# Performance work log

Hardware: AMD Instinct MI355X
Metric: run time of the kernel (lower is better)

The kernel has to match this reference:

```python
import jax, jax.numpy as jnp
import numpy as np

K = 20
EPS_BN = 1e-5

def knn_idx(x, k):
    # x: [B,N,C] -> k nearest neighbor indices [B,N,k] (self included, as in DGCNN)
    sq = jnp.sum(x * x, axis=-1)                       # [B,N]
    inner = jnp.einsum('bnc,bmc->bnm', x, x)           # [B,N,N]
    neg_dist = 2.0 * inner - sq[:, :, None] - sq[:, None, :]
    _, idx = jax.lax.top_k(neg_dist, k)
    return jax.lax.stop_gradient(idx)

def edge_feat(x, idx):
    # x: [B,N,C], idx: [B,N,k] -> [B,N,k,2C] = cat([x_j - x_i, x_i])
    nbr = jax.vmap(lambda xb, ib: xb[ib])(x, idx)      # [B,N,k,C]
    ctr = jnp.broadcast_to(x[:, :, None, :], nbr.shape)
    return jnp.concatenate([nbr - ctr, ctr], axis=-1)

def edge_conv(x, W, g, b, k):
    e = edge_feat(x, knn_idx(x, k))                    # dynamic kNN graph per layer
    h = jnp.einsum('bnkc,cd->bnkd', e, W)              # 1x1 conv2d
    h = h * (g / jnp.sqrt(1.0 + EPS_BN)) + b           # BN eval (mean=0, var=1)
    return jnp.max(jax.nn.leaky_relu(h, 0.2), axis=2)  # max over neighbors -> [B,N,d]

def layer_norm(x, g, b):
    m = jnp.mean(x, axis=-1, keepdims=True)
    v = jnp.var(x, axis=-1, keepdims=True)
    return (x - m) * jax.lax.rsqrt(v + 1e-5) * g + b

def setup_inputs():
    key = jax.random.key(0)
    B, N = 2, 4096
    ks = jax.random.split(key, 16)
    w = lambda i, shape: jax.random.normal(ks[i], shape, jnp.float32) * 0.05
    ones = lambda d: jnp.ones((d,), jnp.float32)
    zeros = lambda d: jnp.zeros((d,), jnp.float32)
    return dict(
        xyz=jax.random.normal(ks[0], (N, 3), jnp.float32),
        scale=jax.random.normal(ks[1], (N, 3), jnp.float32),
        rot=jax.random.normal(ks[2], (N, 4), jnp.float32),
        opacity=jax.random.normal(ks[3], (N, 1), jnp.float32),
        color=jax.random.normal(ks[4], (N, 3), jnp.float32),
        pose=jax.random.normal(ks[5], (B, 75), jnp.float32),
        lbs_weights=jax.random.normal(ks[6], (N, 24), jnp.float32),
        Wc1=w(7, (226, 64)), g1=ones(64), b1=zeros(64),
        Wc2=w(8, (128, 64)), g2=ones(64), b2=zeros(64),
        Wc3=w(9, (128, 128)), g3=ones(128), b3=zeros(128),
        Wc4=w(10, (256, 256)), g4=ones(256), b4=zeros(256),
        Wc5=w(11, (512, 128)), g5=ones(128), b5=zeros(128),
        Wo1=w(12, (128, 128)), bo1=zeros(128), lg1=ones(128), lb1=zeros(128),
        Wo2=w(13, (128, 128)), bo2=zeros(128), lg2=ones(128), lb2=zeros(128),
        Wo3=w(14, (128, 38)), bo3=zeros(38),
    )

def reference(xyz, scale, rot, opacity, color, pose, lbs_weights,
              Wc1, g1, b1, Wc2, g2, b2, Wc3, g3, b3, Wc4, g4, b4, Wc5, g5, b5,
              Wo1, bo1, lg1, lb1, Wo2, bo2, lg2, lb2, Wo3, bo3):
    B, N = pose.shape[0], xyz.shape[0]
    gfeat = jnp.concatenate([xyz, scale, rot, opacity, color], axis=-1)   # [N,14]
    feats = jnp.concatenate([
        jnp.broadcast_to(gfeat[None], (B, N, gfeat.shape[-1])),
        jnp.broadcast_to(lbs_weights[None], (B, N, lbs_weights.shape[-1])),
        jnp.broadcast_to(pose[:, None, :], (B, N, pose.shape[-1])),
    ], axis=-1)                                                            # [B,N,113]
    # DGCNN graph encoder (dynamic kNN EdgeConv stack)
    x1 = edge_conv(feats, Wc1, g1, b1, K)   # [B,N,64]
    x2 = edge_conv(x1, Wc2, g2, b2, K)      # [B,N,64]
    x3 = edge_conv(x2, Wc3, g3, b3, K)      # [B,N,128]
    x4 = edge_conv(x3, Wc4, g4, b4, K)      # [B,N,256]
    cat = jnp.concatenate([x1, x2, x3, x4], axis=-1)                      # [B,N,512]
    gf = jax.nn.leaky_relu(
        jnp.einsum('bnc,cd->bnd', cat, Wc5) * (g5 / jnp.sqrt(1.0 + EPS_BN)) + b5, 0.2)
    # offset predictor MLP
    h = jax.nn.leaky_relu(layer_norm(gf @ Wo1 + bo1, lg1, lb1), 0.2)
    h = jax.nn.leaky_relu(layer_norm(h @ Wo2 + bo2, lg2, lb2), 0.2)
    off = h @ Wo3 + bo3                                                   # [B,N,38]
    # residual add of gaussian offsets (first 14 dims), lbs offsets raw (last 24)
    out = jnp.concatenate([gfeat[None] + off[..., :14], off[..., 14:]], axis=-1)
    return out                                                            # [B,N,38]
```

## Files before the change

kernel.cpp:

```cpp
#include <hip/hip_runtime.h>
#include <math.h>

#define KNN 20
#define BN_INV 0.9999950000374997f

__device__ __forceinline__ unsigned f2o(float f){
    unsigned u = __float_as_uint(f);
    return (u >> 31) ? ~u : (u | 0x80000000u);
}
__device__ __forceinline__ float o2f(unsigned u){
    return __uint_as_float((u >> 31) ? (u & 0x7fffffffu) : ~u);
}
__device__ __forceinline__ float leaky(float v){ return v > 0.f ? v : 0.2f * v; }

__global__ __launch_bounds__(128) void build_feats_kernel(
    const float* __restrict__ xyz, const float* __restrict__ scale,
    const float* __restrict__ rot, const float* __restrict__ opac,
    const float* __restrict__ color, const float* __restrict__ pose,
    const float* __restrict__ lbs, float* __restrict__ feats,
    float* __restrict__ sqout, int N)
{
    __shared__ float sred[2];
    int row = blockIdx.x;
    int b = row / N, n = row % N;
    int c = threadIdx.x;
    float v = 0.f;
    if      (c <   3) v = xyz  [n*3 + c];
    else if (c <   6) v = scale[n*3 + c-3];
    else if (c <  10) v = rot  [n*4 + c-6];
    else if (c <  11) v = opac [n];
    else if (c <  14) v = color[n*3 + c-11];
    else if (c <  38) v = lbs  [n*24 + c-14];
    else if (c < 113) v = pose [b*75 + c-38];
    if (c < 116) feats[(long)row*116 + c] = v;
    float ss = v * v;
    #pragma unroll
    for (int off = 32; off; off >>= 1) ss += __shfl_xor(ss, off);
    if ((c & 63) == 0) sred[c >> 6] = ss;
    __syncthreads();
    if (c == 0) sqout[row] = sred[0] + sred[1];
}


template<int C>
__global__ __launch_bounds__(256) void dist_gemm_kernel(
    const float* __restrict__ x, int N, int CP, float* __restrict__ G)
{
    __shared__ __align__(16) float xi[128][68];
    __shared__ __align__(16) float xj[128][68];
    const int b  = blockIdx.z;
    const int bi = blockIdx.x * 128;
    const int bj = blockIdx.y * 128;
    const int t  = threadIdx.x;
    const int tx = t & 15, ty = t >> 4;
    const int CP4 = CP / 4;
    const long base = (long)b * N;
    const float4* xp = (const float4*)x;

    float acc[8][8] = {};

    for (int c0 = 0; c0 < C; c0 += 64){
        const int KCc = (C - c0 < 64) ? (C - c0) : 64;
        const int KC4 = KCc >> 2;
        __syncthreads();
        for (int f = t; f < 128 * KC4; f += 256){
            int r = f / KC4, c4 = f - r * KC4;
            float4 a = xp[(base + bi + r) * CP4 + (c0 >> 2) + c4];
            float4 bv = xp[(base + bj + r) * CP4 + (c0 >> 2) + c4];
            *(float4*)&xi[r][c4 * 4] = a;
            *(float4*)&xj[r][c4 * 4] = bv;
        }
        __syncthreads();
        for (int c = 0; c < KCc; c += 4){
            float4 A[8], Bv[8];
            #pragma unroll
            for (int ii = 0; ii < 8; ++ii) A[ii]  = *(const float4*)&xi[ty + 16*ii][c];
            #pragma unroll
            for (int jj = 0; jj < 8; ++jj) Bv[jj] = *(const float4*)&xj[tx + 16*jj][c];
            #pragma unroll
            for (int ii = 0; ii < 8; ++ii)
                #pragma unroll
                for (int jj = 0; jj < 8; ++jj){
                    acc[ii][jj] = fmaf(A[ii].x, Bv[jj].x, acc[ii][jj]);
                    acc[ii][jj] = fmaf(A[ii].y, Bv[jj].y, acc[ii][jj]);
                    acc[ii][jj] = fmaf(A[ii].z, Bv[jj].z, acc[ii][jj]);
                    acc[ii][jj] = fmaf(A[ii].w, Bv[jj].w, acc[ii][jj]);
                }
        }
    }

    #pragma unroll
    for (int ii = 0; ii < 8; ++ii){
        long rbase = (base + bi + ty + 16*ii) * N + bj;
        #pragma unroll
        for (int jj = 0; jj < 8; ++jj)
            G[rbase + tx + 16*jj] = acc[ii][jj];
    }
}

#define TCAP 256
__global__ __launch_bounds__(256) void topk_kernel(
    const float* __restrict__ G, const float* __restrict__ sq,
    int N, int* __restrict__ idx_out)
{
    __shared__ unsigned smax[256];
    __shared__ unsigned cand_u[TCAP];
    __shared__ int      cand_j[TCAP];
    __shared__ unsigned cand_cnt;
    __shared__ unsigned sTu;

    const int row = blockIdx.x;
    const int b   = row >> 12;
    const int t   = threadIdx.x;
    const float4* g4  = (const float4*)(G  + (long)row * 4096);
    const float4* sq4 = (const float4*)(sq + (long)b   * 4096);

    unsigned u[16];
    #pragma unroll
    for (int qq = 0; qq < 4; ++qq){
        int v4 = t + 256 * qq;
        float4 gg = g4[v4];
        float4 ss = sq4[v4];
        u[4*qq+0] = f2o(fmaf(2.f, gg.x, -ss.x));
        u[4*qq+1] = f2o(fmaf(2.f, gg.y, -ss.y));
        u[4*qq+2] = f2o(fmaf(2.f, gg.z, -ss.z));
        u[4*qq+3] = f2o(fmaf(2.f, gg.w, -ss.w));
    }

    unsigned mu = u[0];
    #pragma unroll
    for (int q = 1; q < 16; ++q) mu = u[q] > mu ? u[q] : mu;
    smax[t] = mu;
    if (t == 0) cand_cnt = 0;
    __syncthreads();

    int rank = 0;
    for (int k = 0; k < 256; ++k){
        unsigned ou = smax[k];
        rank += (ou > mu) || (ou == mu && k < t);
    }
    if (rank == KNN - 1) sTu = mu;
    __syncthreads();
    const unsigned Tu = sTu;

    #pragma unroll
    for (int qq = 0; qq < 4; ++qq)
        #pragma unroll
        for (int m = 0; m < 4; ++m){
            int q = 4*qq + m;
            if (u[q] >= Tu){
                unsigned p = atomicAdd(&cand_cnt, 1u);
                if (p < TCAP){ cand_u[p] = u[q]; cand_j[p] = 4*(t + 256*qq) + m; }
            }
        }
    __syncthreads();
    const int cc = (int)cand_cnt;

    if (cc <= TCAP){
        if (t < cc){
            unsigned cu = cand_u[t]; int cj = cand_j[t];
            int r = 0;
            for (int k = 0; k < cc; ++k){
                unsigned ou = cand_u[k];
                r += (ou > cu) || (ou == cu && cand_j[k] < cj);
            }
            if (r < KNN) idx_out[(long)row * KNN + r] = cj;
        }
    } else {
        __shared__ unsigned rv[4]; __shared__ int ri[4]; __shared__ int gj_;
        unsigned lv = 0u; int lj = 0x7fffffff;
        #pragma unroll
        for (int q = 0; q < 16; ++q)
            if (u[q] > lv){ lv = u[q]; lj = 4*(t + 256*(q>>2)) + (q&3); }
        for (int it = 0; it < KNN; ++it){
            unsigned bv = lv; int bj = lj;
            #pragma unroll
            for (int off = 32; off; off >>= 1){
                unsigned ov = __shfl_xor(bv, off);
                int      oj = __shfl_xor(bj, off);
                if (ov > bv || (ov == bv && oj < bj)){ bv = ov; bj = oj; }
            }
            if ((t & 63) == 0){ rv[t >> 6] = bv; ri[t >> 6] = bj; }
            __syncthreads();
            if (t == 0){
                unsigned fv = rv[0]; int fj = ri[0];
                #pragma unroll
                for (int w = 1; w < 4; ++w)
                    if (rv[w] > fv || (rv[w] == fv && ri[w] < fj)){ fv = rv[w]; fj = ri[w]; }
                gj_ = fj;
                idx_out[(long)row * KNN + it] = fj;
            }
            __syncthreads();
            int fj = gj_;
            if (fj >= 0 && ((fj >> 2) & 255) == t){
                u[((fj >> 10) << 2) | (fj & 3)] = 0u;
                lv = 0u; lj = 0x7fffffff;
                #pragma unroll
                for (int q = 0; q < 16; ++q)
                    if (u[q] > lv){ lv = u[q]; lj = 4*(t + 256*(q>>2)) + (q&3); }
            }
            __syncthreads();
        }
    }
}


__global__ void prep_wcat_kernel(const float* __restrict__ W, int C, int CP, int D,
                                 float* __restrict__ Wcat)
{
    int i = blockIdx.x * 256 + threadIdx.x;
    int TWOD = 2 * D;
    if (i >= CP * TWOD) return;
    int c = i / TWOD, n = i - c * TWOD;
    float v = 0.f;
    if (c < C) v = (n < D) ? W[c*D + n] : (W[(C + c)*D + (n - D)] - W[c*D + (n - D)]);
    Wcat[i] = v;
}

__global__ __launch_bounds__(256) void gemm_pq_kernel(
    const float* __restrict__ X, int CP, const float* __restrict__ Wcat,
    const float* __restrict__ g, const float* __restrict__ bias,
    int D, int TWOD, float* __restrict__ PQ)
{
    __shared__ __align__(16) float As[128][68];
    __shared__ __align__(16) float Bs[64][132];
    const int bi = blockIdx.x * 128;
    const int bn = blockIdx.y * 128;
    const int t  = threadIdx.x;
    const int tx = t & 15, ty = t >> 4;
    const int CP4 = CP / 4;
    const float4* xp = (const float4*)X;

    float acc[8][8] = {};

    for (int c0 = 0; c0 < CP; c0 += 64){
        const int KC = (CP - c0 < 64) ? (CP - c0) : 64;
        const int KC4 = KC >> 2;
        __syncthreads();
        for (int f = t; f < 128 * KC4; f += 256){
            int r = f / KC4, c4 = f - r * KC4;
            *(float4*)&As[r][c4 * 4] = xp[(long)(bi + r) * CP4 + (c0 >> 2) + c4];
        }
        for (int f = t; f < KC * 32; f += 256){
            int r = f >> 5, c4 = f & 31;
            *(float4*)&Bs[r][c4 * 4] = *(const float4*)&Wcat[(long)(c0 + r) * TWOD + bn + c4 * 4];
        }
        __syncthreads();
        for (int c = 0; c < KC; c += 4){
            float4 A[8];
            #pragma unroll
            for (int ii = 0; ii < 8; ++ii) A[ii] = *(const float4*)&As[ty + 16*ii][c];
            float Bv0[8], Bv1[8], Bv2[8], Bv3[8];
            #pragma unroll
            for (int jj = 0; jj < 8; ++jj){
                Bv0[jj] = Bs[c+0][tx + 16*jj];
                Bv1[jj] = Bs[c+1][tx + 16*jj];
                Bv2[jj] = Bs[c+2][tx + 16*jj];
                Bv3[jj] = Bs[c+3][tx + 16*jj];
            }
            #pragma unroll
            for (int ii = 0; ii < 8; ++ii)
                #pragma unroll
                for (int jj = 0; jj < 8; ++jj){
                    acc[ii][jj] = fmaf(A[ii].x, Bv0[jj], acc[ii][jj]);
                    acc[ii][jj] = fmaf(A[ii].y, Bv1[jj], acc[ii][jj]);
                    acc[ii][jj] = fmaf(A[ii].z, Bv2[jj], acc[ii][jj]);
                    acc[ii][jj] = fmaf(A[ii].w, Bv3[jj], acc[ii][jj]);
                }
        }
    }

    #pragma unroll
    for (int jj = 0; jj < 8; ++jj){
        int n = bn + tx + 16*jj;
        int d = (n < D) ? n : n - D;
        float gg = g[d] * BN_INV;
        float bb = (n < D) ? 0.f : bias[d];
        #pragma unroll
        for (int ii = 0; ii < 8; ++ii)
            PQ[(long)(bi + ty + 16*ii) * TWOD + n] = fmaf(acc[ii][jj], gg, bb);
    }
}

template<int D, int RPB>
__global__ __launch_bounds__(256) void gather_max_kernel(
    const float* __restrict__ PQ, const int* __restrict__ idx, int N,
    float* __restrict__ y, float* __restrict__ sqout)
{
    __shared__ int   lidx[RPB][KNN];
    __shared__ float sred[4];
    const int rb = blockIdx.x * RPB;
    const int t  = threadIdx.x;
    if (t < RPB * KNN) lidx[t / KNN][t % KNN] = idx[(long)rb * KNN + t];
    __syncthreads();

    const int r = t / D, d = t - r * D;
    const int row = rb + r;
    const long base = (long)(row / N) * N;
    const int TWOD = 2 * D;

    float q = PQ[(long)row * TWOD + D + d];
    float m = -INFINITY;
    #pragma unroll
    for (int k = 0; k < KNN; ++k){
        int j = lidx[r][k];
        m = fmaxf(m, PQ[(base + j) * TWOD + d]);
    }
    float val = leaky(m + q);
    y[(long)row * D + d] = val;

    float ss = val * val;
    #pragma unroll
    for (int off = 32; off; off >>= 1) ss += __shfl_xor(ss, off);
    if ((t & 63) == 0) sred[t >> 6] = ss;
    __syncthreads();
    if (d == 0){
        constexpr int WPR = D / 64;
        float s = 0.f;
        int w0 = (r * D) >> 6;
        #pragma unroll
        for (int w = 0; w < WPR; ++w) s += sred[w0 + w];
        sqout[row] = s;
    }
}

__global__ __launch_bounds__(256) void knn_kernel(
    const float* __restrict__ x, int N, int CP4, int* __restrict__ idx_out)
{
    __shared__ float4 xi4[32];
    __shared__ float drow[4096];
    __shared__ float rv[4];
    __shared__ int   ri[4];

    int row = blockIdx.x;
    int b = row / N;
    int t = threadIdx.x;
    const float4* xp = (const float4*)x;

    if (t < CP4) xi4[t] = xp[(long)row * CP4 + t];
    __syncthreads();

    long bb = (long)b * N * CP4;
    for (int j = t; j < N; j += 256){
        const float4* p = xp + bb + (long)j * CP4;
        float acc = 0.f;
        #pragma unroll 4
        for (int c = 0; c < CP4; ++c){
            float4 xv = p[c], yv = xi4[c];
            float dx = xv.x - yv.x, dy = xv.y - yv.y;
            float dz = xv.z - yv.z, dw = xv.w - yv.w;
            acc += dx*dx + dy*dy + dz*dz + dw*dw;
        }
        drow[j] = -acc;
    }
    __syncthreads();

    for (int it = 0; it < KNN; ++it){
        float bv = -INFINITY; int bi = N;
        for (int j = t; j < N; j += 256){
            float v = drow[j];
            if (v > bv){ bv = v; bi = j; }
        }
        #pragma unroll
        for (int off = 32; off > 0; off >>= 1){
            float ov = __shfl_xor(bv, off);
            int   oi = __shfl_xor(bi, off);
            if (ov > bv || (ov == bv && oi < bi)){ bv = ov; bi = oi; }
        }
        if ((t & 63) == 0){ rv[t >> 6] = bv; ri[t >> 6] = bi; }
        __syncthreads();
        if (t == 0){
            float fv = rv[0]; int fi = ri[0];
            #pragma unroll
            for (int w = 1; w < 4; ++w){
                if (rv[w] > fv || (rv[w] == fv && ri[w] < fi)){ fv = rv[w]; fi = ri[w]; }
            }
            idx_out[(long)row * KNN + it] = fi;
            drow[fi] = -INFINITY;
        }
        __syncthreads();
    }
}

template<int D, int KPT>
__global__ __launch_bounds__(256) void edge_conv_kernel(
    const float* __restrict__ x, int N, int C, int CP,
    const float* __restrict__ W, const float* __restrict__ g,
    const float* __restrict__ bias, const int* __restrict__ idx,
    float* __restrict__ y, float* __restrict__ sqout)
{
    __shared__ float xi[128];
    __shared__ float nbr[KNN * 128];
    __shared__ float t2[D];
    __shared__ unsigned um[D];
    __shared__ float sred[4];

    int row = blockIdx.x;
    int b = row / N;
    int t = threadIdx.x;

    for (int c = t; c < C; c += 256) xi[c] = x[(long)row * CP + c];
    for (int kk = 0; kk < KNN; ++kk){
        int j = idx[(long)row * KNN + kk];
        long nb = ((long)b * N + j) * CP;
        for (int c = t; c < C; c += 256) nbr[kk * C + c] = x[nb + c];
    }
    __syncthreads();

    for (int d = t; d < D; d += 256){
        float s = 0.f;
        for (int c = 0; c < C; ++c) s += xi[c] * W[(C + c) * D + d];
        t2[d] = s; um[d] = 0u;
    }
    __syncthreads();

    const int d  = t % D;
    const int kg = t / D;
    float s[KPT];
    #pragma unroll
    for (int q = 0; q < KPT; ++q) s[q] = t2[d];

    const float* nb0 = &nbr[(kg * KPT) * C];
    for (int c = 0; c < C; ++c){
        float w   = W[c * D + d];
        float xic = xi[c];
        #pragma unroll
        for (int q = 0; q < KPT; ++q)
            s[q] += (nb0[q * C + c] - xic) * w;
    }
    float g_ = g[d] * BN_INV, b_ = bias[d];
    float m = -INFINITY;
    #pragma unroll
    for (int q = 0; q < KPT; ++q)
        m = fmaxf(m, leaky(s[q] * g_ + b_));
    atomicMax(&um[d], f2o(m));
    __syncthreads();

    float ss = 0.f;
    for (int dd = t; dd < D; dd += 256){
        float val = o2f(um[dd]);
        y[(long)row * D + dd] = val;
        ss += val * val;
    }
    #pragma unroll
    for (int off = 32; off; off >>= 1) ss += __shfl_xor(ss, off);
    if ((t & 63) == 0) sred[t >> 6] = ss;
    __syncthreads();
    if (t == 0) sqout[row] = sred[0] + sred[1] + sred[2] + sred[3];
}

__global__ __launch_bounds__(128) void head_kernel(
    const float* __restrict__ x1, const float* __restrict__ x2,
    const float* __restrict__ x3, const float* __restrict__ x4,
    const float* __restrict__ feats,
    const float* __restrict__ Wc5, const float* __restrict__ g5, const float* __restrict__ b5,
    const float* __restrict__ Wo1, const float* __restrict__ bo1,
    const float* __restrict__ lg1, const float* __restrict__ lb1,
    const float* __restrict__ Wo2, const float* __restrict__ bo2,
    const float* __restrict__ lg2, const float* __restrict__ lb2,
    const float* __restrict__ Wo3, const float* __restrict__ bo3,
    float* __restrict__ out, int N)
{
    __shared__ float cat[512];
    __shared__ float a[128];
    __shared__ float red[128];
    __shared__ float stats[2];

    int row = blockIdx.x;
    int t = threadIdx.x;

    cat[t]       = (t < 64) ? x1[(long)row*64 + t] : x2[(long)row*64 + (t-64)];
    cat[128 + t] = x3[(long)row*128 + t];
    cat[256 + t] = x4[(long)row*256 + t];
    cat[384 + t] = x4[(long)row*256 + 128 + t];
    __syncthreads();

    float s = 0.f;
    for (int c = 0; c < 512; ++c) s += cat[c] * Wc5[c*128 + t];
    a[t] = leaky(s * g5[t] * BN_INV + b5[t]);
    __syncthreads();

    for (int layer = 0; layer < 2; ++layer){
        const float* W  = layer ? Wo2 : Wo1;
        const float* bo = layer ? bo2 : bo1;
        const float* lg = layer ? lg2 : lg1;
        const float* lb = layer ? lb2 : lb1;
        s = bo[t];
        for (int c = 0; c < 128; ++c) s += a[c] * W[c*128 + t];
        red[t] = s; __syncthreads();
        for (int st = 64; st > 0; st >>= 1){
            if (t < st) red[t] += red[t + st];
            __syncthreads();
        }
        if (t == 0) stats[0] = red[0] * (1.f/128.f);
        __syncthreads();
        float m = stats[0];
        float dm = s - m;
        red[t] = dm * dm; __syncthreads();
        for (int st = 64; st > 0; st >>= 1){
            if (t < st) red[t] += red[t + st];
            __syncthreads();
        }
        if (t == 0) stats[1] = red[0] * (1.f/128.f);
        __syncthreads();
        float var = stats[1];
        float hn = leaky(dm * rsqrtf(var + 1e-5f) * lg[t] + lb[t]);
        __syncthreads();
        a[t] = hn;
        __syncthreads();
    }

    if (t < 38){
        float o = bo3[t];
        for (int c = 0; c < 128; ++c) o += a[c] * Wo3[c*38 + t];
        if (t < 14) o += feats[(long)row*116 + t];
        out[(long)row*38 + t] = o;
    }
}

extern "C" void kernel_launch(void* const* d_in, const int* in_sizes, int n_in,
                              void* d_out, int out_size, void* d_ws, size_t ws_size,
                              hipStream_t stream)
{
    const float* xyz  = (const float*)d_in[0];
    const float* scal = (const float*)d_in[1];
    const float* rot  = (const float*)d_in[2];
    const float* opac = (const float*)d_in[3];
    const float* colr = (const float*)d_in[4];
    const float* pose = (const float*)d_in[5];
    const float* lbs  = (const float*)d_in[6];
    const float* Wc1 = (const float*)d_in[7];  const float* g1 = (const float*)d_in[8];  const float* b1 = (const float*)d_in[9];
    const float* Wc2 = (const float*)d_in[10]; const float* g2 = (const float*)d_in[11]; const float* b2 = (const float*)d_in[12];
    const float* Wc3 = (const float*)d_in[13]; const float* g3 = (const float*)d_in[14]; const float* b3 = (const float*)d_in[15];
    const float* Wc4 = (const float*)d_in[16]; const float* g4 = (const float*)d_in[17]; const float* b4 = (const float*)d_in[18];
    const float* Wc5 = (const float*)d_in[19]; const float* g5 = (const float*)d_in[20]; const float* b5 = (const float*)d_in[21];
    const float* Wo1 = (const float*)d_in[22]; const float* bo1 = (const float*)d_in[23];
    const float* lg1 = (const float*)d_in[24]; const float* lb1 = (const float*)d_in[25];
    const float* Wo2 = (const float*)d_in[26]; const float* bo2 = (const float*)d_in[27];
    const float* lg2 = (const float*)d_in[28]; const float* lb2 = (const float*)d_in[29];
    const float* Wo3 = (const float*)d_in[30]; const float* bo3 = (const float*)d_in[31];

    const int N = in_sizes[0] / 3;
    const int B = in_sizes[5] / 75;
    const int R = B * N;

    char* ws = (char*)d_ws;
    size_t o = 0;
    float* feats = (float*)(ws + o); o += (size_t)R * 116 * 4;
    float* x1    = (float*)(ws + o); o += (size_t)R * 64  * 4;
    float* x2    = (float*)(ws + o); o += (size_t)R * 64  * 4;
    float* x3    = (float*)(ws + o); o += (size_t)R * 128 * 4;
    float* x4    = (float*)(ws + o); o += (size_t)R * 256 * 4;
    int*   idx   = (int*)  (ws + o); o += (size_t)R * KNN * 4;
    float* sq    = (float*)(ws + o); o += (size_t)R * 4;
    float* Wcat  = (float*)(ws + o); o += (size_t)128 * 512 * 4;
    float* G     = (float*)(ws + o);
    float* PQ    = G;
    size_t need  = o + (size_t)B * N * N * 4;

    const bool fast = (N == 4096) && (ws_size >= need);

    build_feats_kernel<<<R, 128, 0, stream>>>(xyz, scal, rot, opac, colr, pose, lbs, feats, sq, N);

    if (fast){
        dim3 gg(N/128, N/128, B);

        dist_gemm_kernel<116><<<gg, 256, 0, stream>>>(feats, N, 116, G);
        topk_kernel<<<R, 256, 0, stream>>>(G, sq, N, idx);
        prep_wcat_kernel<<<(116*128 + 255)/256, 256, 0, stream>>>(Wc1, 113, 116, 64, Wcat);
        gemm_pq_kernel<<<dim3(R/128, 1), 256, 0, stream>>>(feats, 116, Wcat, g1, b1, 64, 128, PQ);
        gather_max_kernel<64, 4><<<R/4, 256, 0, stream>>>(PQ, idx, N, x1, sq);

        dist_gemm_kernel<64><<<gg, 256, 0, stream>>>(x1, N, 64, G);
        topk_kernel<<<R, 256, 0, stream>>>(G, sq, N, idx);
        prep_wcat_kernel<<<(64*128 + 255)/256, 256, 0, stream>>>(Wc2, 64, 64, 64, Wcat);
        gemm_pq_kernel<<<dim3(R/128, 1), 256, 0, stream>>>(x1, 64, Wcat, g2, b2, 64, 128, PQ);
        gather_max_kernel<64, 4><<<R/4, 256, 0, stream>>>(PQ, idx, N, x2, sq);

        dist_gemm_kernel<64><<<gg, 256, 0, stream>>>(x2, N, 64, G);
        topk_kernel<<<R, 256, 0, stream>>>(G, sq, N, idx);
        prep_wcat_kernel<<<(64*256 + 255)/256, 256, 0, stream>>>(Wc3, 64, 64, 128, Wcat);
        gemm_pq_kernel<<<dim3(R/128, 2), 256, 0, stream>>>(x2, 64, Wcat, g3, b3, 128, 256, PQ);
        gather_max_kernel<128, 2><<<R/2, 256, 0, stream>>>(PQ, idx, N, x3, sq);

        dist_gemm_kernel<128><<<gg, 256, 0, stream>>>(x3, N, 128, G);
        topk_kernel<<<R, 256, 0, stream>>>(G, sq, N, idx);
        prep_wcat_kernel<<<(128*512 + 255)/256, 256, 0, stream>>>(Wc4, 128, 128, 256, Wcat);
        gemm_pq_kernel<<<dim3(R/128, 4), 256, 0, stream>>>(x3, 128, Wcat, g4, b4, 256, 512, PQ);
        gather_max_kernel<256, 1><<<R, 256, 0, stream>>>(PQ, idx, N, x4, sq);
    } else {
        knn_kernel<<<R, 256, 0, stream>>>(feats, N, 116/4, idx);
        edge_conv_kernel<64, 5><<<R, 256, 0, stream>>>(feats, N, 113, 116, Wc1, g1, b1, idx, x1, sq);
        knn_kernel<<<R, 256, 0, stream>>>(x1, N, 64/4, idx);
        edge_conv_kernel<64, 5><<<R, 256, 0, stream>>>(x1, N, 64, 64, Wc2, g2, b2, idx, x2, sq);
        knn_kernel<<<R, 256, 0, stream>>>(x2, N, 64/4, idx);
        edge_conv_kernel<128, 10><<<R, 256, 0, stream>>>(x2, N, 64, 64, Wc3, g3, b3, idx, x3, sq);
        knn_kernel<<<R, 256, 0, stream>>>(x3, N, 128/4, idx);
        edge_conv_kernel<256, 20><<<R, 256, 0, stream>>>(x3, N, 128, 128, Wc4, g4, b4, idx, x4, sq);
    }

    head_kernel<<<R, 128, 0, stream>>>(x1, x2, x3, x4, feats,
                                       Wc5, g5, b5, Wo1, bo1, lg1, lb1,
                                       Wo2, bo2, lg2, lb2, Wo3, bo3,
                                       (float*)d_out, N);
}
```

Baseline: 950.0 us.

## Exploit Gram symmetry in distance GEMM and batch rows in head MLP

The distance GEMM now computes only upper-triangular 128x128 tiles and writes each off-diagonal tile a second time, transposed through shared memory, cutting the Gram FLOPs roughly in half. The head kernel processes 8 points per block, so each weight load is reused across 8 rows, and it computes LayerNorm statistics with wave shuffles instead of serial shared-memory tree reductions. The cost is a transposed-write pass, and variance is now E[x^2]-m^2, which is slightly less numerically stable.

```diff
diff --git a/kernel.cpp b/kernel.cpp
--- a/kernel.cpp
+++ b/kernel.cpp
@@ -46,8 +46,11 @@
 __global__ __launch_bounds__(256) void dist_gemm_kernel(
     const float* __restrict__ x, int N, int CP, float* __restrict__ G)
 {
-    __shared__ __align__(16) float xi[128][68];
-    __shared__ __align__(16) float xj[128][68];
+    __shared__ __align__(16) float smem[2*128*68];
+    float (*xi)[68] = (float(*)[68])smem;
+    float (*xj)[68] = (float(*)[68])(smem + 128*68);
+
+    if (blockIdx.y < blockIdx.x) return;
     const int b  = blockIdx.z;
     const int bi = blockIdx.x * 128;
     const int bj = blockIdx.y * 128;
@@ -95,6 +98,24 @@
         #pragma unroll
         for (int jj = 0; jj < 8; ++jj)
             G[rbase + tx + 16*jj] = acc[ii][jj];
+    }
+
+    if (bi != bj){
+        __syncthreads();
+        float (*tr)[132] = (float(*)[132])smem;
+        #pragma unroll
+        for (int ii = 0; ii < 8; ++ii)
+            #pragma unroll
+            for (int jj = 0; jj < 8; ++jj)
+                tr[tx + 16*jj][ty + 16*ii] = acc[ii][jj];
+        __syncthreads();
+        const int r0 = t >> 5;
+        const int cc = (t & 31) * 4;
+        #pragma unroll
+        for (int f = 0; f < 16; ++f){
+            int r = r0 + 8 * f;
+            *(float4*)&G[(base + bj + r) * N + bi + cc] = *(const float4*)&tr[r][cc];
+        }
     }
 }
 
@@ -449,6 +470,7 @@
     if (t == 0) sqout[row] = sred[0] + sred[1] + sred[2] + sred[3];
 }
 
+#define HP 8
 __global__ __launch_bounds__(128) void head_kernel(
     const float* __restrict__ x1, const float* __restrict__ x2,
     const float* __restrict__ x3, const float* __restrict__ x4,
@@ -459,25 +481,50 @@
     const float* __restrict__ Wo2, const float* __restrict__ bo2,
     const float* __restrict__ lg2, const float* __restrict__ lb2,
     const float* __restrict__ Wo3, const float* __restrict__ bo3,
-    float* __restrict__ out, int N)
-{
-    __shared__ float cat[512];
-    __shared__ float a[128];
-    __shared__ float red[128];
-    __shared__ float stats[2];
-
-    int row = blockIdx.x;
-    int t = threadIdx.x;
-
-    cat[t]       = (t < 64) ? x1[(long)row*64 + t] : x2[(long)row*64 + (t-64)];
-    cat[128 + t] = x3[(long)row*128 + t];
-    cat[256 + t] = x4[(long)row*256 + t];
-    cat[384 + t] = x4[(long)row*256 + 128 + t];
-    __syncthreads();
-
-    float s = 0.f;
-    for (int c = 0; c < 512; ++c) s += cat[c] * Wc5[c*128 + t];
-    a[t] = leaky(s * g5[t] * BN_INV + b5[t]);
+    float* __restrict__ out, int N, int R)
+{
+    __shared__ __align__(16) float cat[HP][520];
+    __shared__ __align__(16) float hb[HP][132];
+    __shared__ float wsum[2][HP], wsq[2][HP];
+    __shared__ float f14[HP][14];
+
+    const int t = threadIdx.x;
+    const long p0 = (long)blockIdx.x * HP;
+    const int wid = t >> 6;
+
+    long rows[HP];
+    #pragma unroll
+    for (int p = 0; p < HP; ++p){
+        long row = p0 + p; if (row >= R) row = R - 1;
+        rows[p] = row;
+        cat[p][t]       = (t < 64) ? x1[row*64 + t] : x2[row*64 + (t-64)];
+        cat[p][128 + t] = x3[row*128 + t];
+        cat[p][256 + t] = x4[row*256 + t];
+        cat[p][384 + t] = x4[row*256 + 128 + t];
+        if (t < 14) f14[p][t] = feats[row*116 + t];
+    }
+    __syncthreads();
+
+    const float g5t = g5[t] * BN_INV, b5t = b5[t];
+    float acc[HP];
+    #pragma unroll
+    for (int p = 0; p < HP; ++p) acc[p] = 0.f;
+    for (int c4 = 0; c4 < 128; ++c4){
+        float w0 = Wc5[(4*c4+0)*128 + t];
+        float w1 = Wc5[(4*c4+1)*128 + t];
+        float w2 = Wc5[(4*c4+2)*128 + t];
+        float w3 = Wc5[(4*c4+3)*128 + t];
+        #pragma unroll
+        for (int p = 0; p < HP; ++p){
+            float4 cv = *(const float4*)&cat[p][4*c4];
+            acc[p] = fmaf(cv.x, w0, acc[p]);
+            acc[p] = fmaf(cv.y, w1, acc[p]);
+            acc[p] = fmaf(cv.z, w2, acc[p]);
+            acc[p] = fmaf(cv.w, w3, acc[p]);
+        }
+    }
+    #pragma unroll
+    for (int p = 0; p < HP; ++p) hb[p][t] = leaky(fmaf(acc[p], g5t, b5t));
     __syncthreads();
 
     for (int layer = 0; layer < 2; ++layer){
@@ -485,36 +532,65 @@
         const float* bo = layer ? bo2 : bo1;
         const float* lg = layer ? lg2 : lg1;
         const float* lb = layer ? lb2 : lb1;
-        s = bo[t];
-        for (int c = 0; c < 128; ++c) s += a[c] * W[c*128 + t];
-        red[t] = s; __syncthreads();
-        for (int st = 64; st > 0; st >>= 1){
-            if (t < st) red[t] += red[t + st];
-            __syncthreads();
-        }
-        if (t == 0) stats[0] = red[0] * (1.f/128.f);
-        __syncthreads();
-        float m = stats[0];
-        float dm = s - m;
-        red[t] = dm * dm; __syncthreads();
-        for (int st = 64; st > 0; st >>= 1){
-            if (t < st) red[t] += red[t + st];
-            __syncthreads();
-        }
-        if (t == 0) stats[1] = red[0] * (1.f/128.f);
-        __syncthreads();
-        float var = stats[1];
-        float hn = leaky(dm * rsqrtf(var + 1e-5f) * lg[t] + lb[t]);
-        __syncthreads();
-        a[t] = hn;
+        float a2[HP];
+        float bot = bo[t];
+        #pragma unroll
+        for (int p = 0; p < HP; ++p) a2[p] = bot;
+        for (int c4 = 0; c4 < 32; ++c4){
+            float w0 = W[(4*c4+0)*128 + t];
+            float w1 = W[(4*c4+1)*128 + t];
+            float w2 = W[(4*c4+2)*128 + t];
+            float w3 = W[(4*c4+3)*128 + t];
+            #pragma unroll
+            for (int p = 0; p < HP; ++p){
+                float4 hv = *(const float4*)&hb[p][4*c4];
+                a2[p] = fmaf(hv.x, w0, a2[p]);
+                a2[p] = fmaf(hv.y, w1, a2[p]);
+                a2[p] = fmaf(hv.z, w2, a2[p]);
+                a2[p] = fmaf(hv.w, w3, a2[p]);
+            }
+        }
+        #pragma unroll
+        for (int p = 0; p < HP; ++p){
+            float s1 = a2[p], s2 = a2[p]*a2[p];
+            #pragma unroll
+            for (int off = 32; off; off >>= 1){
+                s1 += __shfl_xor(s1, off);
+                s2 += __shfl_xor(s2, off);
+            }
+            if ((t & 63) == 0){ wsum[wid][p] = s1; wsq[wid][p] = s2; }
+        }
+        __syncthreads();
+        float lgt = lg[t], lbt = lb[t];
+        float hn[HP];
+        #pragma unroll
+        for (int p = 0; p < HP; ++p){
+            float m  = (wsum[0][p] + wsum[1][p]) * (1.f/128.f);
+            float v  = (wsq[0][p]  + wsq[1][p])  * (1.f/128.f) - m*m;
+            float dm = a2[p] - m;
+            hn[p] = leaky(dm * rsqrtf(v + 1e-5f) * lgt + lbt);
+        }
+        __syncthreads();
+        #pragma unroll
+        for (int p = 0; p < HP; ++p) hb[p][t] = hn[p];
         __syncthreads();
     }
 
     if (t < 38){
-        float o = bo3[t];
-        for (int c = 0; c < 128; ++c) o += a[c] * Wo3[c*38 + t];
-        if (t < 14) o += feats[(long)row*116 + t];
-        out[(long)row*38 + t] = o;
+        float o[HP];
+        float bt = bo3[t];
+        #pragma unroll
+        for (int p = 0; p < HP; ++p) o[p] = bt;
+        for (int c = 0; c < 128; ++c){
+            float w = Wo3[c*38 + t];
+            #pragma unroll
+            for (int p = 0; p < HP; ++p) o[p] = fmaf(hb[p][c], w, o[p]);
+        }
+        #pragma unroll
+        for (int p = 0; p < HP; ++p){
+            float val = o[p] + ((t < 14) ? f14[p][t] : 0.f);
+            out[rows[p]*38 + t] = val;
+        }
     }
 }
 
@@ -599,8 +675,8 @@
         edge_conv_kernel<256, 20><<<R, 256, 0, stream>>>(x3, N, 128, 128, Wc4, g4, b4, idx, x4, sq);
     }
 
-    head_kernel<<<R, 128, 0, stream>>>(x1, x2, x3, x4, feats,
+    head_kernel<<<(R + HP - 1)/HP, 128, 0, stream>>>(x1, x2, x3, x4, feats,
                                        Wc5, g5, b5, Wo1, bo1, lg1, lb1,
                                        Wo2, bo2, lg2, lb2, Wo3, bo3,
-                                       (float*)d_out, N);
-}
+                                       (float*)d_out, N, R);
+}
```

Result: no change. 936.2 us (-1.5%).
